# Optimization experiments

Hardware: AMD Instinct MI355X
Metric: run time of the kernel (lower is better)

The kernel has to match this reference:

```python
import math
import jax, jax.numpy as jnp
import numpy as np

N, S, D = 1024, 256, 256
C, R, CLASSES = 256, 64, 1000


def setup_inputs() -> dict:
    key = jax.random.key(0)
    ks = jax.random.split(key, 10)
    inv_sqrt_d = 1.0 / math.sqrt(D)
    return {
        "q": jax.random.normal(ks[0], (N, D), dtype=jnp.float32),
        "K": jax.random.normal(ks[1], (N, S, D), dtype=jnp.float32),
        "V": jax.random.normal(ks[2], (N, S, D), dtype=jnp.float32),
        "codebook": jax.random.normal(ks[3], (C, D), dtype=jnp.float32) * inv_sqrt_d,
        "residual_codebook": jax.random.normal(ks[4], (R, D), dtype=jnp.float32) * inv_sqrt_d,
        "Wq": jax.random.normal(ks[5], (D, D), dtype=jnp.float32) * inv_sqrt_d,
        "residual_logit": jnp.zeros((), dtype=jnp.float32),
        "Wc": jax.random.normal(ks[6], (CLASSES, D), dtype=jnp.float32) * inv_sqrt_d,
        "bc": jnp.zeros((CLASSES,), dtype=jnp.float32),
        "Wr": jax.random.normal(ks[7], (D, D), dtype=jnp.float32) * inv_sqrt_d,
        "br": jnp.zeros((D,), dtype=jnp.float32),
    }


def reference(q, K, V, codebook, residual_codebook, Wq, residual_logit, Wc, bc, Wr, br):
    scale = math.sqrt(q.shape[-1])
    q_proj = q @ Wq.T  # [N,D]

    # --- base codebook pass ---
    code_weights = jax.nn.softmax(jnp.einsum('nd,cd->nc', q_proj, codebook) / scale, axis=-1)
    slot_code_weights = jax.nn.softmax(jnp.einsum('nsd,cd->nsc', K, codebook) / scale, axis=-1)
    slot_code_summaries = jnp.einsum('nsc,nsd->ncd', slot_code_weights, V)
    base_summary = jnp.einsum('nc,ncd->nd', code_weights, slot_code_summaries)
    base_weights = jnp.einsum('nc,nsc->ns', code_weights, slot_code_weights)

    # --- residual quantization pass ---
    query_residual = q_proj - code_weights @ codebook
    slot_residual = K - jnp.einsum('nsc,cd->nsd', slot_code_weights, codebook)
    residual_code_weights = jax.nn.softmax(
        jnp.einsum('nd,rd->nr', query_residual, residual_codebook) / scale, axis=-1)
    residual_slot_code_weights = jax.nn.softmax(
        jnp.einsum('nsd,rd->nsr', slot_residual, residual_codebook) / scale, axis=-1)
    residual_slot_summaries = jnp.einsum('nsr,nsd->nrd', residual_slot_code_weights, V)
    residual_summary = jnp.einsum('nr,nrd->nd', residual_code_weights, residual_slot_summaries)
    residual_weights = jnp.einsum('nr,nsr->ns', residual_code_weights, residual_slot_code_weights)

    gate = jax.nn.sigmoid(residual_logit)
    summary = base_summary + gate * residual_summary
    effective_weights = (base_weights + gate * residual_weights) / (1.0 + gate)

    logits = summary @ Wc.T + bc
    recon = summary @ Wr.T + br
    return (logits, recon, effective_weights)
```

## Files before the change

### kernel.cpp

```cpp
#include <hip/hip_runtime.h>
#include <hip/hip_bf16.h>
#include <math.h>

#define N_   1024
#define S_   256
#define D_   256
#define C_   256
#define R_   64
#define CLS_ 1000
#define INV16 0.0625f

typedef unsigned short ushortT;
typedef unsigned int uint32;
typedef short bf8 __attribute__((ext_vector_type(8)));
typedef float f4 __attribute__((ext_vector_type(4)));

static __device__ __forceinline__ float bf2f(uint32 u){
  return __uint_as_float(u << 16);
}
static __device__ __forceinline__ ushortT f2bf(float f){
  uint32 x = __float_as_uint(f);
  uint32 r = x + 0x7FFFu + ((x >> 16) & 1u);
  return (ushortT)(r >> 16);
}
static __device__ __forceinline__ uint32 packbf(float a, float b){
  return ((uint32)f2bf(b) << 16) | (uint32)f2bf(a);
}
static __device__ __forceinline__ float wred_max(float v){
  for (int o = 32; o; o >>= 1) v = fmaxf(v, __shfl_xor(v, o));
  return v;
}
static __device__ __forceinline__ float wred_sum(float v){
  for (int o = 32; o; o >>= 1) v += __shfl_xor(v, o);
  return v;
}
static __device__ __forceinline__ int swz(int row, int colbyte){
  return row*512 + ((colbyte & ~15) ^ ((row & 7) << 4)) + (colbyte & 15);
}
static __device__ __forceinline__ int pkidx(int row, int col, int nfrag){
  int ks = col >> 5, hi = (col >> 3) & 3, e = col & 7;
  int frag = row >> 4, l15p = row & 15;
  return ((ks*nfrag + frag)*64 + hi*16 + l15p)*8 + e;
}

__global__ __launch_bounds__(256) void k0(const float* __restrict__ cb,
    const float* __restrict__ rcb, const float* __restrict__ Wc,
    const float* __restrict__ Wr, ushortT* __restrict__ a1pk,
    ushortT* __restrict__ Wcr_bf)
{
  int t = blockIdx.x*256 + threadIdx.x;
  int stride = gridDim.x*256;
  for (int e = t; e < (C_ + R_)*D_; e += stride){
    int row = e >> 8, col = e & 255;
    float v = (row < C_) ? cb[e] : rcb[e - C_*D_];
    a1pk[pkidx(row, col, 20)] = f2bf(v);
  }
  for (int e = t; e < CLS_*D_; e += stride) Wcr_bf[e] = f2bf(Wc[e]);
  for (int e = t; e < D_*D_; e += stride)  Wcr_bf[CLS_*D_ + e] = f2bf(Wr[e]);
  for (int e = t; e < 24*D_; e += stride)  Wcr_bf[1256*D_ + e] = 0;
}

__global__ __launch_bounds__(256) void k0m(const float* __restrict__ cb,
    const float* __restrict__ rcb, float* __restrict__ MT_f32,
    ushortT* __restrict__ mtpk)
{
  __shared__ float rl[D_];
  int r = blockIdx.x;
  int t = threadIdx.x;
  rl[t] = rcb[r*D_ + t];
  __syncthreads();
  float acc = 0.f;
  const float* crow = cb + t*D_;
  #pragma unroll 8
  for (int k = 0; k < D_; k += 4){
    float4 w = *(const float4*)(crow + k);
    acc += w.x*rl[k] + w.y*rl[k+1] + w.z*rl[k+2] + w.w*rl[k+3];
  }
  MT_f32[r*C_ + t] = acc;
  mtpk[pkidx(r, t, 4)] = f2bf(acc);
}

__global__ __launch_bounds__(256) void k1(const float* __restrict__ q,
    const float* __restrict__ cb, const float* __restrict__ rcb,
    const float* __restrict__ Wq, const float* __restrict__ MT_f32,
    float* __restrict__ cw_ws, float* __restrict__ rcw_ws)
{
  __shared__ float qv[D_], qp[D_], red[8], redB[8], cwl[C_];
  int n = blockIdx.x, t = threadIdx.x;
  qv[t] = q[n*D_ + t];
  __syncthreads();
  {
    float acc = 0.f;
    const float* wrow = Wq + t*D_;
    #pragma unroll 8
    for (int k = 0; k < D_; k += 4){
      float4 w = *(const float4*)(wrow + k);
      acc += qv[k]*w.x + qv[k+1]*w.y + qv[k+2]*w.z + qv[k+3]*w.w;
    }
    qp[t] = acc;
  }
  __syncthreads();
  float L = 0.f;
  {
    const float* crow = cb + t*D_;
    #pragma unroll 8
    for (int k = 0; k < D_; k += 4){
      float4 w = *(const float4*)(crow + k);
      L += qp[k]*w.x + qp[k+1]*w.y + qp[k+2]*w.z + qp[k+3]*w.w;
    }
    L *= INV16;
  }
  float m = wred_max(L);
  if ((t & 63) == 0) red[t >> 6] = m;
  __syncthreads();
  m = fmaxf(fmaxf(red[0], red[1]), fmaxf(red[2], red[3]));
  float e = __expf(L - m);
  float s = wred_sum(e);
  if ((t & 63) == 0) redB[t >> 6] = s;
  __syncthreads();
  s = redB[0] + redB[1] + redB[2] + redB[3];
  float w = e / s;
  cwl[t] = w;
  cw_ws[n*C_ + t] = w;
  __syncthreads();
  if (t < R_){
    float qdot = 0.f, mdot = 0.f;
    const float* rrow = rcb + t*D_;
    const float* mrow = MT_f32 + t*C_;
    #pragma unroll 8
    for (int k = 0; k < D_; k += 4){
      float4 wv = *(const float4*)(rrow + k);
      qdot += qp[k]*wv.x + qp[k+1]*wv.y + qp[k+2]*wv.z + qp[k+3]*wv.w;
      float4 mv = *(const float4*)(mrow + k);
      mdot += cwl[k]*mv.x + cwl[k+1]*mv.y + cwl[k+2]*mv.z + cwl[k+3]*mv.w;
    }
    float Lr = (qdot - mdot) * INV16;
    float mr = wred_max(Lr);
    float er = __expf(Lr - mr);
    float sr = wred_sum(er);
    rcw_ws[n*R_ + t] = er / sr;
  }
}

__global__ __launch_bounds__(256, 2) void k2(const float* __restrict__ Kt,
    const float* __restrict__ Vt, const ushortT* __restrict__ a1pk,
    const ushortT* __restrict__ mtpk, const float* __restrict__ cw_ws,
    const float* __restrict__ rcw_ws, const float* __restrict__ rlogit,
    float* __restrict__ sum_ws, float* __restrict__ out_ew)
{
  __shared__ __align__(16) ushortT KW[64*256];
  __shared__ __align__(16) ushortT MTl[16384];
  __shared__ float redS[4][64], redW[4][64];
  __shared__ float cwl[C_], rcwl[R_];

  int bx  = blockIdx.x;
  int n   = bx >> 2;
  int s0  = (bx & 3) * 64;
  int tid = threadIdx.x;
  int lane = tid & 63, w = tid >> 6;
  int l15 = lane & 15, l4 = lane >> 4;
  int sabs = w*16 + l15;
  float gate  = 1.f / (1.f + __expf(-rlogit[0]));
  float inv1g = 1.f / (1.f + gate);

  const float* Kn = Kt + (size_t)n * S_ * D_ + (size_t)s0 * D_;
  const float* Vn = Vt + (size_t)n * S_ * D_ + (size_t)s0 * D_;

  if (tid < C_) cwl[tid]  = cw_ws[n*C_ + tid];
  if (tid < R_) rcwl[tid] = rcw_ws[n*R_ + tid];

  #pragma unroll
  for (int j = 0; j < 8; j++)
    *(uint4*)(&MTl[(size_t)(tid + j*256)*8]) =
        *(const uint4*)(mtpk + (size_t)(tid + j*256)*8);
  #pragma unroll
  for (int j = 0; j < 8; j++){
    int ch = tid + j*256;
    int row = ch >> 5, blk = ch & 31;
    const float* src = Kn + row*D_ + blk*8;
    float4 a = *(const float4*)src;
    float4 b = *(const float4*)(src + 4);
    uint4 wv = {packbf(a.x,a.y), packbf(a.z,a.w), packbf(b.x,b.y), packbf(b.z,b.w)};
    *(uint4*)((char*)KW + swz(row, blk*16)) = wv;
  }
  __syncthreads();

  float cw_r[16];
  #pragma unroll
  for (int f = 0; f < 4; f++)
    #pragma unroll
    for (int rg = 0; rg < 4; rg++)
      cw_r[f*4+rg] = cwl[(w + 4*f)*16 + l4*4 + rg];
  float rcw_r[4];
  #pragma unroll
  for (int rg = 0; rg < 4; rg++) rcw_r[rg] = rcwl[w*16 + l4*4 + rg];

  const ushortT* a1w = a1pk + (size_t)(w*64 + lane)*8;
  bf8 bnx[5];
  #pragma unroll
  for (int f = 0; f < 5; f++)
    bnx[f] = *(const bf8*)(a1w + (size_t)(4*f)*512);
  f4 acc[5][4];
  #pragma unroll
  for (int f = 0; f < 5; f++)
    #pragma unroll
    for (int sj = 0; sj < 4; sj++) acc[f][sj] = (f4)0.f;
  #pragma unroll
  for (int ks = 0; ks < 8; ks++){
    bf8 bcur[5];
    #pragma unroll
    for (int f = 0; f < 5; f++) bcur[f] = bnx[f];
    if (ks < 7){
      #pragma unroll
      for (int f = 0; f < 5; f++)
        bnx[f] = *(const bf8*)(a1w + (size_t)((ks+1)*20 + 4*f)*512);
    }
    bf8 kf[4];
    #pragma unroll
    for (int sj = 0; sj < 4; sj++)
      kf[sj] = *(const bf8*)((const char*)KW + swz(sj*16 + l15, ks*64 + l4*16));
    #pragma unroll
    for (int f = 0; f < 5; f++)
      #pragma unroll
      for (int sj = 0; sj < 4; sj++)
        acc[f][sj] = __builtin_amdgcn_mfma_f32_16x16x32_bf16(bcur[f], kf[sj], acc[f][sj], 0, 0, 0);
  }

  float se[4] = {0,0,0,0}, sb[4] = {0,0,0,0};
  #pragma unroll
  for (int f = 0; f < 4; f++)
    #pragma unroll
    for (int sj = 0; sj < 4; sj++)
      #pragma unroll
      for (int rg = 0; rg < 4; rg++){
        float e = __expf(acc[f][sj][rg] * INV16);
        acc[f][sj][rg] = e;
        se[sj] += e;
        sb[sj] += e * cw_r[f*4+rg];
      }
  #pragma unroll
  for (int sj = 0; sj < 4; sj++){
    se[sj] += __shfl_xor(se[sj], 16); se[sj] += __shfl_xor(se[sj], 32);
    sb[sj] += __shfl_xor(sb[sj], 16); sb[sj] += __shfl_xor(sb[sj], 32);
  }
  if (l4 == 0){
    #pragma unroll
    for (int sj = 0; sj < 4; sj++){
      redS[w][sj*16 + l15] = se[sj];
      redW[w][sj*16 + l15] = sb[sj];
    }
  }
  __syncthreads();
  float rcp[4];
  #pragma unroll
  for (int sj = 0; sj < 4; sj++){
    int s_ = sj*16 + l15;
    rcp[sj] = 1.f / (redS[0][s_] + redS[1][s_] + redS[2][s_] + redS[3][s_]);
  }
  float bw_loc;
  {
    float sS = redS[0][sabs] + redS[1][sabs] + redS[2][sabs] + redS[3][sabs];
    float sW = redW[0][sabs] + redW[1][sabs] + redW[2][sabs] + redW[3][sabs];
    bw_loc = sW / sS;
  }
  #pragma unroll
  for (int f = 0; f < 4; f++){
    int cbyte = ((w + 4*f)*16 + l4*4) * 2;
    #pragma unroll
    for (int sj = 0; sj < 4; sj++){
      int s_ = sj*16 + l15;
      float r = rcp[sj];
      *(uint32*)((char*)KW + swz(s_, cbyte))     = packbf(acc[f][sj][0]*r, acc[f][sj][1]*r);
      *(uint32*)((char*)KW + swz(s_, cbyte + 4)) = packbf(acc[f][sj][2]*r, acc[f][sj][3]*r);
    }
  }
  __syncthreads();

  f4 wmacc[4];
  #pragma unroll
  for (int sj = 0; sj < 4; sj++) wmacc[sj] = (f4)0.f;
  #pragma unroll
  for (int ks = 0; ks < 8; ks++){
    bf8 a = *(const bf8*)(&MTl[(size_t)((ks*4 + w)*64 + lane)*8]);
    #pragma unroll
    for (int sj = 0; sj < 4; sj++){
      bf8 b = *(const bf8*)((const char*)KW + swz(sj*16 + l15, ks*64 + l4*16));
      wmacc[sj] = __builtin_amdgcn_mfma_f32_16x16x32_bf16(a, b, wmacc[sj], 0, 0, 0);
    }
  }

  float se3[4] = {0,0,0,0}, sc3[4] = {0,0,0,0};
  #pragma unroll
  for (int sj = 0; sj < 4; sj++)
    #pragma unroll
    for (int rg = 0; rg < 4; rg++){
      float e = __expf((acc[4][sj][rg] - wmacc[sj][rg]) * INV16);
      se3[sj] += e;
      sc3[sj] += e * rcw_r[rg];
    }
  #pragma unroll
  for (int sj = 0; sj < 4; sj++){
    se3[sj] += __shfl_xor(se3[sj], 16); se3[sj] += __shfl_xor(se3[sj], 32);
    sc3[sj] += __shfl_xor(sc3[sj], 16); sc3[sj] += __shfl_xor(sc3[sj], 32);
  }
  if (l4 == 0){
    #pragma unroll
    for (int sj = 0; sj < 4; sj++){
      redS[w][sj*16 + l15] = se3[sj];
      redW[w][sj*16 + l15] = sc3[sj];
    }
  }
  __syncthreads();
  float comb;
  {
    float sS = redS[0][sabs] + redS[1][sabs] + redS[2][sabs] + redS[3][sabs];
    float sW = redW[0][sabs] + redW[1][sabs] + redW[2][sabs] + redW[3][sabs];
    comb = bw_loc + gate * (sW / sS);
    if (l4 == 0) out_ew[n*S_ + s0 + sabs] = comb * inv1g;
  }

  {
    float4 sacc = {0.f, 0.f, 0.f, 0.f};
    const float* vp = Vn + (size_t)(w*16)*D_ + lane*4;
    #pragma unroll
    for (int j = 0; j < 16; j++){
      float cj = __shfl(comb, j);
      float4 v = *(const float4*)(vp + (size_t)j*D_);
      sacc.x = fmaf(cj, v.x, sacc.x); sacc.y = fmaf(cj, v.y, sacc.y);
      sacc.z = fmaf(cj, v.z, sacc.z); sacc.w = fmaf(cj, v.w, sacc.w);
    }
    float4* sred = (float4*)KW;
    sred[w*64 + lane] = sacc;
  }
  __syncthreads();
  if (tid < 64){
    float4 a0 = ((float4*)KW)[tid],       a1 = ((float4*)KW)[64 + tid];
    float4 a2 = ((float4*)KW)[128 + tid], a3 = ((float4*)KW)[192 + tid];
    float* dst = sum_ws + (size_t)n*D_ + tid*4;
    atomicAdd(dst + 0, a0.x + a1.x + a2.x + a3.x);
    atomicAdd(dst + 1, a0.y + a1.y + a2.y + a3.y);
    atomicAdd(dst + 2, a0.z + a1.z + a2.z + a3.z);
    atomicAdd(dst + 3, a0.w + a1.w + a2.w + a3.w);
  }
}

__global__ __launch_bounds__(256) void k3(const float* __restrict__ sum_ws,
    const ushortT* __restrict__ Wcr_bf, const float* __restrict__ bc,
    const float* __restrict__ br, float* __restrict__ out)
{
  __shared__ __align__(16) ushortT Stile[64*256];
  int bx = blockIdx.x;
  int ot = bx >> 4;
  int nt = bx & 15;
  int tid = threadIdx.x;
  int lane = tid & 63, wid = tid >> 6;
  int l15 = lane & 15, l4 = lane >> 4;

  const float* Sp = sum_ws + (size_t)nt*64*D_;
  #pragma unroll
  for (int j = 0; j < 8; j++){
    int ch = tid + j*256;
    int row = ch >> 5, blk = ch & 31;
    const float* src = Sp + row*D_ + blk*8;
    float4 a = *(const float4*)src;
    float4 b = *(const float4*)(src + 4);
    uint4 wv = {packbf(a.x,a.y), packbf(a.z,a.w), packbf(b.x,b.y), packbf(b.z,b.w)};
    *(uint4*)((char*)Stile + swz(row, blk*16)) = wv;
  }
  __syncthreads();

  int o0 = ot*64 + wid*16;
  const ushortT* Ap = Wcr_bf + (size_t)(o0 + l15)*D_ + l4*8;
  f4 acc[4];
  #pragma unroll
  for (int j = 0; j < 4; j++) acc[j] = (f4)0.f;
  #pragma unroll
  for (int k = 0; k < 8; k++){
    bf8 a = *(const bf8*)(Ap + k*32);
    #pragma unroll
    for (int nj = 0; nj < 4; nj++){
      bf8 b = *(const bf8*)((const char*)Stile + swz(nj*16 + l15, k*64 + l4*16));
      acc[nj] = __builtin_amdgcn_mfma_f32_16x16x32_bf16(a, b, acc[nj], 0, 0, 0);
    }
  }
  int obase = o0 + l4*4;
  if (obase < 1256){
    float4 bias;
    if (obase < CLS_) bias = *(const float4*)(bc + obase);
    else              bias = *(const float4*)(br + (obase - CLS_));
    #pragma unroll
    for (int nj = 0; nj < 4; nj++){
      int nn = nt*64 + nj*16 + l15;
      float4 v = {acc[nj][0]+bias.x, acc[nj][1]+bias.y, acc[nj][2]+bias.z, acc[nj][3]+bias.w};
      if (obase < CLS_) *(float4*)(out + (size_t)nn*CLS_ + obase) = v;
      else              *(float4*)(out + (size_t)N_*CLS_ + (size_t)nn*D_ + (obase - CLS_)) = v;
    }
  }
}

extern "C" void kernel_launch(void* const* d_in, const int* in_sizes, int n_in,
                              void* d_out, int out_size, void* d_ws, size_t ws_size,
                              hipStream_t stream)
{
  const float* q    = (const float*)d_in[0];
  const float* Kt   = (const float*)d_in[1];
  const float* Vt   = (const float*)d_in[2];
  const float* cb   = (const float*)d_in[3];
  const float* rcb  = (const float*)d_in[4];
  const float* Wq   = (const float*)d_in[5];
  const float* rlg  = (const float*)d_in[6];
  const float* Wc   = (const float*)d_in[7];
  const float* bc   = (const float*)d_in[8];
  const float* Wr   = (const float*)d_in[9];
  const float* br   = (const float*)d_in[10];
  float* out = (float*)d_out;
  float* ws  = (float*)d_ws;

  float* cw_ws  = ws;
  float* rcw_ws = ws + 262144;
  float* sum_ws = ws + 327680;
  float* MT_f32 = ws + 589824;
  ushortT* a1pk   = (ushortT*)(ws + 606208);
  ushortT* mtpk   = a1pk + (C_ + R_)*D_;
  ushortT* Wcr_bf = mtpk + R_*C_;

  float* out_logits = out;
  float* out_ew     = out + (size_t)N_*CLS_ + (size_t)N_*D_;

  hipMemsetAsync(sum_ws, 0, (size_t)N_*D_*sizeof(float), stream);
  k0 <<<128,  256, 0, stream>>>(cb, rcb, Wc, Wr, a1pk, Wcr_bf);
  k0m<<<R_,   256, 0, stream>>>(cb, rcb, MT_f32, mtpk);
  k1 <<<N_,   256, 0, stream>>>(q, cb, rcb, Wq, MT_f32, cw_ws, rcw_ws);
  k2 <<<N_*4, 256, 0, stream>>>(Kt, Vt, a1pk, mtpk, cw_ws, rcw_ws, rlg,
                                sum_ws, out_ew);
  k3 <<<320,  256, 0, stream>>>(sum_ws, Wcr_bf, bc, br, out_logits);
}
```

Before: 257.7 us.

## Split slot kernel, batch query rows, fuse prep kernels, drop atomics

Merges the codebook-product prep kernel into the conversion kernel, and makes k1 handle four query rows per block so Wq and codebook loads are reused. The slot kernel now splits each wave's work so it owns its own 16 slots for the residual logits, and applies the softmax normalisation as a scalar after the MFMA instead of before. It reads mtpk from global memory rather than staging it in LDS. The V-weighted reduction moves into a new per-row kernel that writes sums directly, removing the memset and the atomics at the cost of one extra launch and a round trip through a comb buffer.

```diff
diff --git a/kernel.cpp b/kernel.cpp
--- a/kernel.cpp
+++ b/kernel.cpp
@@ -46,112 +46,132 @@
 __global__ __launch_bounds__(256) void k0(const float* __restrict__ cb,
     const float* __restrict__ rcb, const float* __restrict__ Wc,
     const float* __restrict__ Wr, ushortT* __restrict__ a1pk,
-    ushortT* __restrict__ Wcr_bf)
-{
-  int t = blockIdx.x*256 + threadIdx.x;
+    ushortT* __restrict__ Wcr_bf, float* __restrict__ MT_f32,
+    ushortT* __restrict__ mtpk)
+{
+  __shared__ float rl[D_];
+  int bid = blockIdx.x, t = threadIdx.x;
+  int gtid = bid*256 + t;
   int stride = gridDim.x*256;
-  for (int e = t; e < (C_ + R_)*D_; e += stride){
+  for (int e = gtid; e < (C_ + R_)*D_; e += stride){
     int row = e >> 8, col = e & 255;
     float v = (row < C_) ? cb[e] : rcb[e - C_*D_];
     a1pk[pkidx(row, col, 20)] = f2bf(v);
   }
-  for (int e = t; e < CLS_*D_; e += stride) Wcr_bf[e] = f2bf(Wc[e]);
-  for (int e = t; e < D_*D_; e += stride)  Wcr_bf[CLS_*D_ + e] = f2bf(Wr[e]);
-  for (int e = t; e < 24*D_; e += stride)  Wcr_bf[1256*D_ + e] = 0;
-}
-
-__global__ __launch_bounds__(256) void k0m(const float* __restrict__ cb,
-    const float* __restrict__ rcb, float* __restrict__ MT_f32,
-    ushortT* __restrict__ mtpk)
-{
-  __shared__ float rl[D_];
-  int r = blockIdx.x;
-  int t = threadIdx.x;
-  rl[t] = rcb[r*D_ + t];
-  __syncthreads();
-  float acc = 0.f;
-  const float* crow = cb + t*D_;
-  #pragma unroll 8
-  for (int k = 0; k < D_; k += 4){
-    float4 w = *(const float4*)(crow + k);
-    acc += w.x*rl[k] + w.y*rl[k+1] + w.z*rl[k+2] + w.w*rl[k+3];
-  }
-  MT_f32[r*C_ + t] = acc;
-  mtpk[pkidx(r, t, 4)] = f2bf(acc);
-}
-
+  for (int e = gtid; e < CLS_*D_; e += stride) Wcr_bf[e] = f2bf(Wc[e]);
+  for (int e = gtid; e < D_*D_; e += stride)  Wcr_bf[CLS_*D_ + e] = f2bf(Wr[e]);
+  for (int e = gtid; e < 24*D_; e += stride)  Wcr_bf[1256*D_ + e] = 0;
+
+  if (bid < R_){
+    rl[t] = rcb[bid*D_ + t];
+    __syncthreads();
+    float acc = 0.f;
+    const float* crow = cb + t*D_;
+    #pragma unroll 8
+    for (int k = 0; k < D_; k += 4){
+      float4 w = *(const float4*)(crow + k);
+      acc += w.x*rl[k] + w.y*rl[k+1] + w.z*rl[k+2] + w.w*rl[k+3];
+    }
+    MT_f32[bid*C_ + t] = acc;
+    mtpk[pkidx(bid, t, 4)] = f2bf(acc);
+  }
+}
+
+#define G4 4
 __global__ __launch_bounds__(256) void k1(const float* __restrict__ q,
     const float* __restrict__ cb, const float* __restrict__ rcb,
     const float* __restrict__ Wq, const float* __restrict__ MT_f32,
     float* __restrict__ cw_ws, float* __restrict__ rcw_ws)
 {
-  __shared__ float qv[D_], qp[D_], red[8], redB[8], cwl[C_];
-  int n = blockIdx.x, t = threadIdx.x;
-  qv[t] = q[n*D_ + t];
+  __shared__ float qv[G4][D_], qp[G4][D_], cwl[G4][C_];
+  __shared__ float redA[G4][4], redB2[G4][4];
+  int n0 = blockIdx.x*G4, t = threadIdx.x;
+  #pragma unroll
+  for (int g = 0; g < G4; g++) qv[g][t] = q[(n0+g)*D_ + t];
   __syncthreads();
   {
-    float acc = 0.f;
+    float acc[G4] = {0.f,0.f,0.f,0.f};
     const float* wrow = Wq + t*D_;
-    #pragma unroll 8
+    #pragma unroll 4
     for (int k = 0; k < D_; k += 4){
       float4 w = *(const float4*)(wrow + k);
-      acc += qv[k]*w.x + qv[k+1]*w.y + qv[k+2]*w.z + qv[k+3]*w.w;
-    }
-    qp[t] = acc;
-  }
-  __syncthreads();
-  float L = 0.f;
+      #pragma unroll
+      for (int g = 0; g < G4; g++)
+        acc[g] += qv[g][k]*w.x + qv[g][k+1]*w.y + qv[g][k+2]*w.z + qv[g][k+3]*w.w;
+    }
+    #pragma unroll
+    for (int g = 0; g < G4; g++) qp[g][t] = acc[g];
+  }
+  __syncthreads();
+  float L[G4] = {0.f,0.f,0.f,0.f};
   {
     const float* crow = cb + t*D_;
-    #pragma unroll 8
+    #pragma unroll 4
     for (int k = 0; k < D_; k += 4){
       float4 w = *(const float4*)(crow + k);
-      L += qp[k]*w.x + qp[k+1]*w.y + qp[k+2]*w.z + qp[k+3]*w.w;
-    }
-    L *= INV16;
-  }
-  float m = wred_max(L);
-  if ((t & 63) == 0) red[t >> 6] = m;
-  __syncthreads();
-  m = fmaxf(fmaxf(red[0], red[1]), fmaxf(red[2], red[3]));
-  float e = __expf(L - m);
-  float s = wred_sum(e);
-  if ((t & 63) == 0) redB[t >> 6] = s;
-  __syncthreads();
-  s = redB[0] + redB[1] + redB[2] + redB[3];
-  float w = e / s;
-  cwl[t] = w;
-  cw_ws[n*C_ + t] = w;
+      #pragma unroll
+      for (int g = 0; g < G4; g++)
+        L[g] += qp[g][k]*w.x + qp[g][k+1]*w.y + qp[g][k+2]*w.z + qp[g][k+3]*w.w;
+    }
+  }
+  float m[G4], e[G4], s[G4];
+  #pragma unroll
+  for (int g = 0; g < G4; g++){ L[g] *= INV16; m[g] = wred_max(L[g]); }
+  if ((t & 63) == 0)
+    #pragma unroll
+    for (int g = 0; g < G4; g++) redA[g][t >> 6] = m[g];
+  __syncthreads();
+  #pragma unroll
+  for (int g = 0; g < G4; g++){
+    m[g] = fmaxf(fmaxf(redA[g][0], redA[g][1]), fmaxf(redA[g][2], redA[g][3]));
+    e[g] = __expf(L[g] - m[g]);
+    s[g] = wred_sum(e[g]);
+  }
+  if ((t & 63) == 0)
+    #pragma unroll
+    for (int g = 0; g < G4; g++) redB2[g][t >> 6] = s[g];
+  __syncthreads();
+  #pragma unroll
+  for (int g = 0; g < G4; g++){
+    float ss = redB2[g][0] + redB2[g][1] + redB2[g][2] + redB2[g][3];
+    float w = e[g] / ss;
+    cwl[g][t] = w;
+    cw_ws[(n0+g)*C_ + t] = w;
+  }
   __syncthreads();
   if (t < R_){
-    float qdot = 0.f, mdot = 0.f;
+    float qd[G4] = {0.f,0.f,0.f,0.f}, md[G4] = {0.f,0.f,0.f,0.f};
     const float* rrow = rcb + t*D_;
     const float* mrow = MT_f32 + t*C_;
-    #pragma unroll 8
+    #pragma unroll 4
     for (int k = 0; k < D_; k += 4){
       float4 wv = *(const float4*)(rrow + k);
-      qdot += qp[k]*wv.x + qp[k+1]*wv.y + qp[k+2]*wv.z + qp[k+3]*wv.w;
       float4 mv = *(const float4*)(mrow + k);
-      mdot += cwl[k]*mv.x + cwl[k+1]*mv.y + cwl[k+2]*mv.z + cwl[k+3]*mv.w;
-    }
-    float Lr = (qdot - mdot) * INV16;
-    float mr = wred_max(Lr);
-    float er = __expf(Lr - mr);
-    float sr = wred_sum(er);
-    rcw_ws[n*R_ + t] = er / sr;
-  }
-}
-
-__global__ __launch_bounds__(256, 2) void k2(const float* __restrict__ Kt,
-    const float* __restrict__ Vt, const ushortT* __restrict__ a1pk,
-    const ushortT* __restrict__ mtpk, const float* __restrict__ cw_ws,
-    const float* __restrict__ rcw_ws, const float* __restrict__ rlogit,
-    float* __restrict__ sum_ws, float* __restrict__ out_ew)
+      #pragma unroll
+      for (int g = 0; g < G4; g++){
+        qd[g] += qp[g][k]*wv.x + qp[g][k+1]*wv.y + qp[g][k+2]*wv.z + qp[g][k+3]*wv.w;
+        md[g] += cwl[g][k]*mv.x + cwl[g][k+1]*mv.y + cwl[g][k+2]*mv.z + cwl[g][k+3]*mv.w;
+      }
+    }
+    #pragma unroll
+    for (int g = 0; g < G4; g++){
+      float Lr = (qd[g] - md[g]) * INV16;
+      float mr = wred_max(Lr);
+      float er = __expf(Lr - mr);
+      float sr = wred_sum(er);
+      rcw_ws[(n0+g)*R_ + t] = er / sr;
+    }
+  }
+}
+
+__global__ __launch_bounds__(256) void k2a(const float* __restrict__ Kt,
+    const ushortT* __restrict__ a1pk, const ushortT* __restrict__ mtpk,
+    const float* __restrict__ cw_ws, const float* __restrict__ rcw_ws,
+    const float* __restrict__ rlogit, float* __restrict__ comb_ws,
+    float* __restrict__ out_ew)
 {
   __shared__ __align__(16) ushortT KW[64*256];
-  __shared__ __align__(16) ushortT MTl[16384];
   __shared__ float redS[4][64], redW[4][64];
-  __shared__ float cwl[C_], rcwl[R_];
 
   int bx  = blockIdx.x;
   int n   = bx >> 2;
@@ -159,20 +179,11 @@
   int tid = threadIdx.x;
   int lane = tid & 63, w = tid >> 6;
   int l15 = lane & 15, l4 = lane >> 4;
-  int sabs = w*16 + l15;
   float gate  = 1.f / (1.f + __expf(-rlogit[0]));
   float inv1g = 1.f / (1.f + gate);
 
-  const float* Kn = Kt + (size_t)n * S_ * D_ + (size_t)s0 * D_;
-  const float* Vn = Vt + (size_t)n * S_ * D_ + (size_t)s0 * D_;
-
-  if (tid < C_) cwl[tid]  = cw_ws[n*C_ + tid];
-  if (tid < R_) rcwl[tid] = rcw_ws[n*R_ + tid];
-
-  #pragma unroll
-  for (int j = 0; j < 8; j++)
-    *(uint4*)(&MTl[(size_t)(tid + j*256)*8]) =
-        *(const uint4*)(mtpk + (size_t)(tid + j*256)*8);
+  const float* Kn = Kt + (size_t)n*S_*D_ + (size_t)s0*D_;
+
   #pragma unroll
   for (int j = 0; j < 8; j++){
     int ch = tid + j*256;
@@ -185,59 +196,60 @@
   }
   __syncthreads();
 
-  float cw_r[16];
+  const ushortT* a1b = a1pk + (size_t)lane*8;
+  bf8 bnxC[4], bnxR[4];
+  #pragma unroll
+  for (int f = 0; f < 4; f++){
+    bnxC[f] = *(const bf8*)(a1b + (size_t)((w + 4*f)*64)*8);
+    bnxR[f] = *(const bf8*)(a1b + (size_t)((16 + f)*64)*8);
+  }
+  f4 accC[4][4]; f4 accR[4];
+  #pragma unroll
+  for (int f = 0; f < 4; f++){
+    accR[f] = (f4)0.f;
+    #pragma unroll
+    for (int sj = 0; sj < 4; sj++) accC[f][sj] = (f4)0.f;
+  }
+  #pragma unroll
+  for (int ks = 0; ks < 8; ks++){
+    bf8 kf0 = *(const bf8*)((const char*)KW + swz(     l15, ks*64 + l4*16));
+    bf8 kf1 = *(const bf8*)((const char*)KW + swz(16 + l15, ks*64 + l4*16));
+    bf8 kf2 = *(const bf8*)((const char*)KW + swz(32 + l15, ks*64 + l4*16));
+    bf8 kf3 = *(const bf8*)((const char*)KW + swz(48 + l15, ks*64 + l4*16));
+    bf8 kfw = *(const bf8*)((const char*)KW + swz(w*16 + l15, ks*64 + l4*16));
+    #pragma unroll
+    for (int f = 0; f < 4; f++){
+      bf8 aC = bnxC[f], aR = bnxR[f];
+      if (ks < 7){
+        bnxC[f] = *(const bf8*)(a1b + (size_t)(((ks+1)*20 + w + 4*f)*64)*8);
+        bnxR[f] = *(const bf8*)(a1b + (size_t)(((ks+1)*20 + 16 + f)*64)*8);
+      }
+      accC[f][0] = __builtin_amdgcn_mfma_f32_16x16x32_bf16(aC, kf0, accC[f][0], 0, 0, 0);
+      accC[f][1] = __builtin_amdgcn_mfma_f32_16x16x32_bf16(aC, kf1, accC[f][1], 0, 0, 0);
+      accC[f][2] = __builtin_amdgcn_mfma_f32_16x16x32_bf16(aC, kf2, accC[f][2], 0, 0, 0);
+      accC[f][3] = __builtin_amdgcn_mfma_f32_16x16x32_bf16(aC, kf3, accC[f][3], 0, 0, 0);
+      accR[f]    = __builtin_amdgcn_mfma_f32_16x16x32_bf16(aR, kfw, accR[f],    0, 0, 0);
+    }
+  }
+
+  float4 cwv[4];
   #pragma unroll
   for (int f = 0; f < 4; f++)
-    #pragma unroll
-    for (int rg = 0; rg < 4; rg++)
-      cw_r[f*4+rg] = cwl[(w + 4*f)*16 + l4*4 + rg];
-  float rcw_r[4];
-  #pragma unroll
-  for (int rg = 0; rg < 4; rg++) rcw_r[rg] = rcwl[w*16 + l4*4 + rg];
-
-  const ushortT* a1w = a1pk + (size_t)(w*64 + lane)*8;
-  bf8 bnx[5];
-  #pragma unroll
-  for (int f = 0; f < 5; f++)
-    bnx[f] = *(const bf8*)(a1w + (size_t)(4*f)*512);
-  f4 acc[5][4];
-  #pragma unroll
-  for (int f = 0; f < 5; f++)
-    #pragma unroll
-    for (int sj = 0; sj < 4; sj++) acc[f][sj] = (f4)0.f;
-  #pragma unroll
-  for (int ks = 0; ks < 8; ks++){
-    bf8 bcur[5];
-    #pragma unroll
-    for (int f = 0; f < 5; f++) bcur[f] = bnx[f];
-    if (ks < 7){
-      #pragma unroll
-      for (int f = 0; f < 5; f++)
-        bnx[f] = *(const bf8*)(a1w + (size_t)((ks+1)*20 + 4*f)*512);
-    }
-    bf8 kf[4];
-    #pragma unroll
-    for (int sj = 0; sj < 4; sj++)
-      kf[sj] = *(const bf8*)((const char*)KW + swz(sj*16 + l15, ks*64 + l4*16));
-    #pragma unroll
-    for (int f = 0; f < 5; f++)
-      #pragma unroll
-      for (int sj = 0; sj < 4; sj++)
-        acc[f][sj] = __builtin_amdgcn_mfma_f32_16x16x32_bf16(bcur[f], kf[sj], acc[f][sj], 0, 0, 0);
-  }
-
+    cwv[f] = *(const float4*)(cw_ws + n*C_ + (w + 4*f)*16 + l4*4);
   float se[4] = {0,0,0,0}, sb[4] = {0,0,0,0};
   #pragma unroll
   for (int f = 0; f < 4; f++)
     #pragma unroll
-    for (int sj = 0; sj < 4; sj++)
-      #pragma unroll
-      for (int rg = 0; rg < 4; rg++){
-        float e = __expf(acc[f][sj][rg] * INV16);
-        acc[f][sj][rg] = e;
-        se[sj] += e;
-        sb[sj] += e * cw_r[f*4+rg];
-      }
+    for (int sj = 0; sj < 4; sj++){
+      float e0 = __expf(accC[f][sj][0] * INV16);
+      float e1 = __expf(accC[f][sj][1] * INV16);
+      float e2 = __expf(accC[f][sj][2] * INV16);
+      float e3 = __expf(accC[f][sj][3] * INV16);
+      accC[f][sj][0] = e0; accC[f][sj][1] = e1;
+      accC[f][sj][2] = e2; accC[f][sj][3] = e3;
+      se[sj] += (e0 + e1) + (e2 + e3);
+      sb[sj] += e0*cwv[f].x + e1*cwv[f].y + e2*cwv[f].z + e3*cwv[f].w;
+    }
   #pragma unroll
   for (int sj = 0; sj < 4; sj++){
     se[sj] += __shfl_xor(se[sj], 16); se[sj] += __shfl_xor(se[sj], 32);
@@ -251,17 +263,14 @@
     }
   }
   __syncthreads();
-  float rcp[4];
-  #pragma unroll
-  for (int sj = 0; sj < 4; sj++){
-    int s_ = sj*16 + l15;
-    rcp[sj] = 1.f / (redS[0][s_] + redS[1][s_] + redS[2][s_] + redS[3][s_]);
-  }
-  float bw_loc;
+
+  float bw_q, rcp_q;
   {
-    float sS = redS[0][sabs] + redS[1][sabs] + redS[2][sabs] + redS[3][sabs];
-    float sW = redW[0][sabs] + redW[1][sabs] + redW[2][sabs] + redW[3][sabs];
-    bw_loc = sW / sS;
+    int sq = w*16 + l15;
+    float sS = redS[0][sq] + redS[1][sq] + redS[2][sq] + redS[3][sq];
+    float sW = redW[0][sq] + redW[1][sq] + redW[2][sq] + redW[3][sq];
+    bw_q  = sW / sS;
+    rcp_q = 1.f / sS;
   }
   #pragma unroll
   for (int f = 0; f < 4; f++){
@@ -269,78 +278,84 @@
     #pragma unroll
     for (int sj = 0; sj < 4; sj++){
       int s_ = sj*16 + l15;
-      float r = rcp[sj];
-      *(uint32*)((char*)KW + swz(s_, cbyte))     = packbf(acc[f][sj][0]*r, acc[f][sj][1]*r);
-      *(uint32*)((char*)KW + swz(s_, cbyte + 4)) = packbf(acc[f][sj][2]*r, acc[f][sj][3]*r);
-    }
-  }
-  __syncthreads();
-
-  f4 wmacc[4];
-  #pragma unroll
-  for (int sj = 0; sj < 4; sj++) wmacc[sj] = (f4)0.f;
+      *(uint32*)((char*)KW + swz(s_, cbyte))     = packbf(accC[f][sj][0], accC[f][sj][1]);
+      *(uint32*)((char*)KW + swz(s_, cbyte + 4)) = packbf(accC[f][sj][2], accC[f][sj][3]);
+    }
+  }
+  __syncthreads();
+
+  const ushortT* mtb = mtpk + (size_t)lane*8;
+  bf8 mnx[4];
+  #pragma unroll
+  for (int fr = 0; fr < 4; fr++)
+    mnx[fr] = *(const bf8*)(mtb + (size_t)(fr*64)*8);
+  f4 wm[4];
+  #pragma unroll
+  for (int fr = 0; fr < 4; fr++) wm[fr] = (f4)0.f;
   #pragma unroll
   for (int ks = 0; ks < 8; ks++){
-    bf8 a = *(const bf8*)(&MTl[(size_t)((ks*4 + w)*64 + lane)*8]);
-    #pragma unroll
-    for (int sj = 0; sj < 4; sj++){
-      bf8 b = *(const bf8*)((const char*)KW + swz(sj*16 + l15, ks*64 + l4*16));
-      wmacc[sj] = __builtin_amdgcn_mfma_f32_16x16x32_bf16(a, b, wmacc[sj], 0, 0, 0);
-    }
-  }
-
-  float se3[4] = {0,0,0,0}, sc3[4] = {0,0,0,0};
-  #pragma unroll
-  for (int sj = 0; sj < 4; sj++)
-    #pragma unroll
-    for (int rg = 0; rg < 4; rg++){
-      float e = __expf((acc[4][sj][rg] - wmacc[sj][rg]) * INV16);
-      se3[sj] += e;
-      sc3[sj] += e * rcw_r[rg];
-    }
-  #pragma unroll
-  for (int sj = 0; sj < 4; sj++){
-    se3[sj] += __shfl_xor(se3[sj], 16); se3[sj] += __shfl_xor(se3[sj], 32);
-    sc3[sj] += __shfl_xor(sc3[sj], 16); sc3[sj] += __shfl_xor(sc3[sj], 32);
-  }
+    bf8 wb = *(const bf8*)((const char*)KW + swz(w*16 + l15, ks*64 + l4*16));
+    #pragma unroll
+    for (int fr = 0; fr < 4; fr++){
+      bf8 a = mnx[fr];
+      if (ks < 7) mnx[fr] = *(const bf8*)(mtb + (size_t)(((ks+1)*4 + fr)*64)*8);
+      wm[fr] = __builtin_amdgcn_mfma_f32_16x16x32_bf16(a, wb, wm[fr], 0, 0, 0);
+    }
+  }
+
+  float4 rcwv[4];
+  #pragma unroll
+  for (int fr = 0; fr < 4; fr++)
+    rcwv[fr] = *(const float4*)(rcw_ws + n*R_ + fr*16 + l4*4);
+  float se3 = 0.f, sc3 = 0.f;
+  #pragma unroll
+  for (int fr = 0; fr < 4; fr++){
+    float e0 = __expf((accR[fr][0] - wm[fr][0]*rcp_q) * INV16);
+    float e1 = __expf((accR[fr][1] - wm[fr][1]*rcp_q) * INV16);
+    float e2 = __expf((accR[fr][2] - wm[fr][2]*rcp_q) * INV16);
+    float e3 = __expf((accR[fr][3] - wm[fr][3]*rcp_q) * INV16);
+    se3 += (e0 + e1) + (e2 + e3);
+    sc3 += e0*rcwv[fr].x + e1*rcwv[fr].y + e2*rcwv[fr].z + e3*rcwv[fr].w;
+  }
+  se3 += __shfl_xor(se3, 16); se3 += __shfl_xor(se3, 32);
+  sc3 += __shfl_xor(sc3, 16); sc3 += __shfl_xor(sc3, 32);
+  float comb = bw_q + gate * (sc3 / se3);
   if (l4 == 0){
-    #pragma unroll
-    for (int sj = 0; sj < 4; sj++){
-      redS[w][sj*16 + l15] = se3[sj];
-      redW[w][sj*16 + l15] = sc3[sj];
-    }
-  }
-  __syncthreads();
-  float comb;
-  {
-    float sS = redS[0][sabs] + redS[1][sabs] + redS[2][sabs] + redS[3][sabs];
-    float sW = redW[0][sabs] + redW[1][sabs] + redW[2][sabs] + redW[3][sabs];
-    comb = bw_loc + gate * (sW / sS);
-    if (l4 == 0) out_ew[n*S_ + s0 + sabs] = comb * inv1g;
-  }
-
-  {
-    float4 sacc = {0.f, 0.f, 0.f, 0.f};
-    const float* vp = Vn + (size_t)(w*16)*D_ + lane*4;
-    #pragma unroll
-    for (int j = 0; j < 16; j++){
-      float cj = __shfl(comb, j);
-      float4 v = *(const float4*)(vp + (size_t)j*D_);
-      sacc.x = fmaf(cj, v.x, sacc.x); sacc.y = fmaf(cj, v.y, sacc.y);
-      sacc.z = fmaf(cj, v.z, sacc.z); sacc.w = fmaf(cj, v.w, sacc.w);
-    }
-    float4* sred = (float4*)KW;
-    sred[w*64 + lane] = sacc;
-  }
+    int sabs = n*S_ + s0 + w*16 + l15;
+    out_ew[sabs]  = comb * inv1g;
+    comb_ws[sabs] = comb;
+  }
+}
+
+__global__ __launch_bounds__(256) void k2b(const float* __restrict__ Vt,
+    const float* __restrict__ comb_ws, float* __restrict__ sum_ws)
+{
+  __shared__ float cl[S_];
+  __shared__ float4 part[4][64];
+  int n = blockIdx.x, tid = threadIdx.x;
+  int lane = tid & 63, w = tid >> 6;
+  cl[tid] = comb_ws[n*S_ + tid];
+  __syncthreads();
+  const float* Vn = Vt + (size_t)n*S_*D_ + (size_t)(w*64)*D_ + lane*4;
+  float4 a0 = {0,0,0,0}, a1 = {0,0,0,0};
+  #pragma unroll 8
+  for (int j = 0; j < 64; j += 2){
+    float4 v0 = *(const float4*)(Vn + (size_t)j*D_);
+    float4 v1 = *(const float4*)(Vn + (size_t)(j+1)*D_);
+    float c0 = cl[w*64 + j], c1 = cl[w*64 + j + 1];
+    a0.x = fmaf(c0, v0.x, a0.x); a0.y = fmaf(c0, v0.y, a0.y);
+    a0.z = fmaf(c0, v0.z, a0.z); a0.w = fmaf(c0, v0.w, a0.w);
+    a1.x = fmaf(c1, v1.x, a1.x); a1.y = fmaf(c1, v1.y, a1.y);
+    a1.z = fmaf(c1, v1.z, a1.z); a1.w = fmaf(c1, v1.w, a1.w);
+  }
+  float4 acc = {a0.x+a1.x, a0.y+a1.y, a0.z+a1.z, a0.w+a1.w};
+  part[w][lane] = acc;
   __syncthreads();
   if (tid < 64){
-    float4 a0 = ((float4*)KW)[tid],       a1 = ((float4*)KW)[64 + tid];
-    float4 a2 = ((float4*)KW)[128 + tid], a3 = ((float4*)KW)[192 + tid];
-    float* dst = sum_ws + (size_t)n*D_ + tid*4;
-    atomicAdd(dst + 0, a0.x + a1.x + a2.x + a3.x);
-    atomicAdd(dst + 1, a0.y + a1.y + a2.y + a3.y);
-    atomicAdd(dst + 2, a0.z + a1.z + a2.z + a3.z);
-    atomicAdd(dst + 3, a0.w + a1.w + a2.w + a3.w);
+    float4 p0 = part[0][tid], p1 = part[1][tid], p2 = part[2][tid], p3 = part[3][tid];
+    float4 r = {p0.x+p1.x+p2.x+p3.x, p0.y+p1.y+p2.y+p3.y,
+                p0.z+p1.z+p2.z+p3.z, p0.w+p1.w+p2.w+p3.w};
+    *(float4*)(sum_ws + (size_t)n*D_ + tid*4) = r;
   }
 }
 
@@ -416,22 +431,21 @@
   float* out = (float*)d_out;
   float* ws  = (float*)d_ws;
 
-  float* cw_ws  = ws;
-  float* rcw_ws = ws + 262144;
-  float* sum_ws = ws + 327680;
-  float* MT_f32 = ws + 589824;
-  ushortT* a1pk   = (ushortT*)(ws + 606208);
+  float* cw_ws   = ws;
+  float* rcw_ws  = ws + 262144;
+  float* sum_ws  = ws + 327680;
+  float* comb_ws = ws + 589824;
+  float* MT_f32  = ws + 851968;
+  ushortT* a1pk   = (ushortT*)(ws + 868352);
   ushortT* mtpk   = a1pk + (C_ + R_)*D_;
   ushortT* Wcr_bf = mtpk + R_*C_;
 
   float* out_logits = out;
   float* out_ew     = out + (size_t)N_*CLS_ + (size_t)N_*D_;
 
-  hipMemsetAsync(sum_ws, 0, (size_t)N_*D_*sizeof(float), stream);
-  k0 <<<128,  256, 0, stream>>>(cb, rcb, Wc, Wr, a1pk, Wcr_bf);
-  k0m<<<R_,   256, 0, stream>>>(cb, rcb, MT_f32, mtpk);
-  k1 <<<N_,   256, 0, stream>>>(q, cb, rcb, Wq, MT_f32, cw_ws, rcw_ws);
-  k2 <<<N_*4, 256, 0, stream>>>(Kt, Vt, a1pk, mtpk, cw_ws, rcw_ws, rlg,
-                                sum_ws, out_ew);
-  k3 <<<320,  256, 0, stream>>>(sum_ws, Wcr_bf, bc, br, out_logits);
-}
+  k0 <<<128,   256, 0, stream>>>(cb, rcb, Wc, Wr, a1pk, Wcr_bf, MT_f32, mtpk);
+  k1 <<<N_/G4, 256, 0, stream>>>(q, cb, rcb, Wq, MT_f32, cw_ws, rcw_ws);
+  k2a<<<N_*4,  256, 0, stream>>>(Kt, a1pk, mtpk, cw_ws, rcw_ws, rlg, comb_ws, out_ew);
+  k2b<<<N_,    256, 0, stream>>>(Vt, comb_ws, sum_ws);
+  k3 <<<320,   256, 0, stream>>>(sum_ws, Wcr_bf, bc, br, out_logits);
+}
```

Result: faster. 234.4 us (-9.0%).
